# Kernel tuning notes

Measured on AMD Instinct MI355X. Metric: run time of the kernel, lower is better.

Reference implementation:

```python
import jax, jax.numpy as jnp
import numpy as np

B, L, C, H = 8, 2048, 1024, 16
HID = 4 * C


def _rope(x):
    # Faithful to source: rotation angle depends only on feature index (no position scaling).
    b, n, c = x.shape
    k_max = c // 2
    theta = 1.0 / (10000.0 ** (jnp.arange(k_max, dtype=jnp.float32) / k_max))
    cos_t, sin_t = jnp.cos(theta), jnp.sin(theta)
    xr = x.reshape(b, n, k_max, 2)
    re = xr[..., 0] * cos_t - xr[..., 1] * sin_t
    im = xr[..., 0] * sin_t + xr[..., 1] * cos_t
    return jnp.stack((re, im), axis=-1).reshape(b, n, c)


def _dwconv(x_bcl, w, bias):
    # depthwise conv1d, kernel 3, padding 1; w: (C,1,3)
    y = jax.lax.conv_general_dilated(
        x_bcl, w, (1,), [(1, 1)],
        dimension_numbers=('NCH', 'OIH', 'NCH'),
        feature_group_count=x_bcl.shape[1])
    return y + bias[None, :, None]


def _ln(x, g, b, eps=1e-5):
    mu = x.mean(-1, keepdims=True)
    var = ((x - mu) ** 2).mean(-1, keepdims=True)
    return (x - mu) * jax.lax.rsqrt(var + eps) * g + b


def _mlla_forward(x, cpe1_w, cpe1_b, norm1_g, norm1_b, in_w, in_b, actp_w, actp_b,
                  dwc_w, dwc_b, qk_w, qk_b, lepe_w, lepe_b, out_w, out_b,
                  cpe2_w, cpe2_b, norm2_g, norm2_b, fc1_w, fc1_b, fc2_w, fc2_b):
    b, n, c = x.shape
    h, d = H, c // H
    # cpe1 residual
    x = x + _dwconv(x.transpose(0, 2, 1), cpe1_w, cpe1_b).transpose(0, 2, 1)
    shortcut = x
    xn = _ln(x, norm1_g, norm1_b)
    act_res = jax.nn.silu(xn @ actp_w + actp_b)
    xi = xn @ in_w + in_b
    xi = jax.nn.silu(_dwconv(xi.transpose(0, 2, 1), dwc_w, dwc_b)).transpose(0, 2, 1)
    # linear attention with ELU+1 feature map and RoPE on q/k
    qk = xi @ qk_w + qk_b                       # (b,n,2c)
    q = jax.nn.elu(qk[..., :c]) + 1.0
    k = jax.nn.elu(qk[..., c:]) + 1.0
    q_rope = _rope(q).reshape(b, n, h, d).transpose(0, 2, 1, 3)  # (b,h,n,d)
    k_rope = _rope(k).reshape(b, n, h, d).transpose(0, 2, 1, 3)
    qh = q.reshape(b, n, h, d).transpose(0, 2, 1, 3)
    kh = k.reshape(b, n, h, d).transpose(0, 2, 1, 3)
    vh = xi.reshape(b, n, h, d).transpose(0, 2, 1, 3)
    k_mean = kh.mean(axis=2, keepdims=True)                      # (b,h,1,d)
    z = 1.0 / (jnp.einsum('bhnd,bhmd->bhnm', qh, k_mean) + 1e-6)  # (b,h,n,1)
    kv = jnp.einsum('bhnd,bhne->bhde', k_rope, vh) * (1.0 / n)   # (k*n^-0.5)^T @ (v*n^-0.5)
    attn = jnp.einsum('bhnd,bhde->bhne', q_rope, kv) * z         # (b,h,n,d)
    attn = attn.transpose(0, 2, 1, 3).reshape(b, n, c)
    v_bcl = vh.transpose(0, 2, 1, 3).reshape(b, n, c).transpose(0, 2, 1)
    attn = attn + _dwconv(v_bcl, lepe_w, lepe_b).transpose(0, 2, 1)
    # gated output projection + residual
    x = shortcut + (attn * act_res) @ out_w + out_b
    # cpe2 residual
    x = x + _dwconv(x.transpose(0, 2, 1), cpe2_w, cpe2_b).transpose(0, 2, 1)
    # MLP (exact GELU, as torch default)
    xn2 = _ln(x, norm2_g, norm2_b)
    mlp = jax.nn.gelu(xn2 @ fc1_w + fc1_b, approximate=False) @ fc2_w + fc2_b
    return x + mlp


def setup_inputs() -> dict:
    key = jax.random.key(0)
    ks = jax.random.split(key, 12)
    def nrm(k, shape, scale=0.02):
        return jax.random.normal(k, shape, jnp.float32) * scale
    return {
        'x': jax.random.normal(ks[0], (B, L, C), jnp.float32),
        'cpe1_w': nrm(ks[1], (C, 1, 3), 0.1), 'cpe1_b': jnp.zeros((C,), jnp.float32),
        'norm1_g': jnp.ones((C,), jnp.float32), 'norm1_b': jnp.zeros((C,), jnp.float32),
        'in_w': nrm(ks[2], (C, C)), 'in_b': jnp.zeros((C,), jnp.float32),
        'actp_w': nrm(ks[3], (C, C)), 'actp_b': jnp.zeros((C,), jnp.float32),
        'dwc_w': nrm(ks[4], (C, 1, 3), 0.1), 'dwc_b': jnp.zeros((C,), jnp.float32),
        'qk_w': nrm(ks[5], (C, 2 * C)), 'qk_b': jnp.zeros((2 * C,), jnp.float32),
        'lepe_w': nrm(ks[6], (C, 1, 3), 0.1), 'lepe_b': jnp.zeros((C,), jnp.float32),
        'out_w': nrm(ks[7], (C, C)), 'out_b': jnp.zeros((C,), jnp.float32),
        'cpe2_w': nrm(ks[8], (C, 1, 3), 0.1), 'cpe2_b': jnp.zeros((C,), jnp.float32),
        'norm2_g': jnp.ones((C,), jnp.float32), 'norm2_b': jnp.zeros((C,), jnp.float32),
        'fc1_w': nrm(ks[9], (C, HID)), 'fc1_b': jnp.zeros((HID,), jnp.float32),
        'fc2_w': nrm(ks[10], (HID, C)), 'fc2_b': jnp.zeros((C,), jnp.float32),
    }


def reference(x, cpe1_w, cpe1_b, norm1_g, norm1_b, in_w, in_b, actp_w, actp_b,
              dwc_w, dwc_b, qk_w, qk_b, lepe_w, lepe_b, out_w, out_b,
              cpe2_w, cpe2_b, norm2_g, norm2_b, fc1_w, fc1_b, fc2_w, fc2_b):
    return _mlla_forward(x, cpe1_w, cpe1_b, norm1_g, norm1_b, in_w, in_b, actp_w, actp_b,
                         dwc_w, dwc_b, qk_w, qk_b, lepe_w, lepe_b, out_w, out_b,
                         cpe2_w, cpe2_b, norm2_g, norm2_b, fc1_w, fc1_b, fc2_w, fc2_b)
```

## Files before the change

kernel.cpp:

```cpp
#include <hip/hip_runtime.h>
#include <hip/hip_bf16.h>
#include <cstdint>

#define B_    8
#define L_    2048
#define C_    1024
#define H_    16
#define D_    64
#define BL_   16384
#define C2_   2048
#define HID_  4096
#define KMAX_ 512

typedef unsigned short u16;
typedef unsigned int   u32;
typedef __attribute__((ext_vector_type(8))) short short8;
typedef __attribute__((ext_vector_type(4))) float f32x4;
typedef __attribute__((ext_vector_type(16))) float f32x16;

__device__ __forceinline__ u16 f2bf(float f){
  u32 u = __float_as_uint(f);
  u += 0x7fffu + ((u >> 16) & 1u);
  return (u16)(u >> 16);
}
__device__ __forceinline__ float bf2f(u16 v){
  return __uint_as_float(((u32)v) << 16);
}
__device__ __forceinline__ void gld16(const void* g, void* l){
  __builtin_amdgcn_global_load_lds((const __attribute__((address_space(1))) u32*)g,
                                   (__attribute__((address_space(3))) u32*)l, 16, 0, 0);
}

__global__ __launch_bounds__(256) void zerofill_kernel(float* __restrict__ p, int n){
  int i = blockIdx.x * 256 + threadIdx.x;
  if (i < n) p[i] = 0.f;
}

__global__ __launch_bounds__(256) void concat_bias_kernel(
    const float* __restrict__ b0, const float* __restrict__ b1, float* __restrict__ o){
  int i = blockIdx.x * 256 + threadIdx.x;
  if (i < C_) o[i] = b0[i];
  else if (i < C2_) o[i] = b1[i - C_];
}

__global__ void rope_table_kernel(float* __restrict__ cosS, float* __restrict__ sinS){
  int t = threadIdx.x;
  if (t < KMAX_){
    float th = powf(10000.f, -(float)t / (float)KMAX_);
    cosS[t] = cosf(th);
    sinS[t] = sinf(th);
  }
}

__global__ __launch_bounds__(256) void transpose_bf16_kernel(
    const float* __restrict__ in, u16* __restrict__ out, int R, int Ccol)
{
  __shared__ float tile[32][33];
  int tx = threadIdx.x & 31, ty = threadIdx.x >> 5;
  int c = blockIdx.x * 32 + tx;
  #pragma unroll
  for (int i = 0; i < 4; ++i){
    int r = blockIdx.y * 32 + ty + i * 8;
    tile[ty + i * 8][tx] = in[(size_t)r * Ccol + c];
  }
  __syncthreads();
  int rr = blockIdx.y * 32 + tx;
  #pragma unroll
  for (int i = 0; i < 4; ++i){
    int cc = blockIdx.x * 32 + ty + i * 8;
    out[(size_t)cc * R + rr] = f2bf(tile[tx][ty + i * 8]);
  }
}

template<typename T>
__global__ __launch_bounds__(256) void cpe_ln_kernel(
    const T* __restrict__ xin, const float* __restrict__ cw, const float* __restrict__ cb,
    const float* __restrict__ g,   const float* __restrict__ beta,
    u16* __restrict__ xout, u16* __restrict__ xnout)
{
  int bl = blockIdx.x;
  int l  = bl & (L_ - 1);
  const T* xr = xin + (size_t)bl * C_;
  int t = threadIdx.x;
  float vals[4];
  float s = 0.f, ss = 0.f;
  #pragma unroll
  for (int i = 0; i < 4; ++i){
    int c = t + i * 256;
    float xm = (l > 0)      ? (float)xr[c - C_] : 0.f;
    float x0 = (float)xr[c];
    float xp = (l < L_ - 1) ? (float)xr[c + C_] : 0.f;
    float v = x0 + xm * cw[c*3] + x0 * cw[c*3+1] + xp * cw[c*3+2] + cb[c];
    vals[i] = v; s += v; ss += v * v;
  }
  int lane = t & 63, w = t >> 6;
  #pragma unroll
  for (int o = 32; o > 0; o >>= 1){ s += __shfl_down(s, o); ss += __shfl_down(ss, o); }
  __shared__ float red[8];
  __shared__ float sh[2];
  if (lane == 0){ red[w] = s; red[4 + w] = ss; }
  __syncthreads();
  if (t == 0){
    float S  = red[0] + red[1] + red[2] + red[3];
    float SS = red[4] + red[5] + red[6] + red[7];
    float mu = S * (1.f / C_);
    float var = SS * (1.f / C_) - mu * mu;
    sh[0] = mu; sh[1] = rsqrtf(var + 1e-5f);
  }
  __syncthreads();
  float mu = sh[0], inv = sh[1];
  #pragma unroll
  for (int i = 0; i < 4; ++i){
    int c = t + i * 256;
    float xn = (vals[i] - mu) * inv * g[c] + beta[c];
    xout[(size_t)bl * C_ + c]  = f2bf(vals[i]);
    xnout[(size_t)bl * C_ + c] = f2bf(xn);
  }
}
template<> __global__ __launch_bounds__(256) void cpe_ln_kernel<u16>(
    const u16* __restrict__ xin, const float* __restrict__ cw, const float* __restrict__ cb,
    const float* __restrict__ g,   const float* __restrict__ beta,
    u16* __restrict__ xout, u16* __restrict__ xnout)
{
  int bl = blockIdx.x;
  int l  = bl & (L_ - 1);
  const u16* xr = xin + (size_t)bl * C_;
  int t = threadIdx.x;
  float vals[4];
  float s = 0.f, ss = 0.f;
  #pragma unroll
  for (int i = 0; i < 4; ++i){
    int c = t + i * 256;
    float xm = (l > 0)      ? bf2f(xr[c - C_]) : 0.f;
    float x0 = bf2f(xr[c]);
    float xp = (l < L_ - 1) ? bf2f(xr[c + C_]) : 0.f;
    float v = x0 + xm * cw[c*3] + x0 * cw[c*3+1] + xp * cw[c*3+2] + cb[c];
    vals[i] = v; s += v; ss += v * v;
  }
  int lane = t & 63, w = t >> 6;
  #pragma unroll
  for (int o = 32; o > 0; o >>= 1){ s += __shfl_down(s, o); ss += __shfl_down(ss, o); }
  __shared__ float red[8];
  __shared__ float sh[2];
  if (lane == 0){ red[w] = s; red[4 + w] = ss; }
  __syncthreads();
  if (t == 0){
    float S  = red[0] + red[1] + red[2] + red[3];
    float SS = red[4] + red[5] + red[6] + red[7];
    float mu = S * (1.f / C_);
    float var = SS * (1.f / C_) - mu * mu;
    sh[0] = mu; sh[1] = rsqrtf(var + 1e-5f);
  }
  __syncthreads();
  float mu = sh[0], inv = sh[1];
  #pragma unroll
  for (int i = 0; i < 4; ++i){
    int c = t + i * 256;
    float xn = (vals[i] - mu) * inv * g[c] + beta[c];
    xout[(size_t)bl * C_ + c]  = f2bf(vals[i]);
    xnout[(size_t)bl * C_ + c] = f2bf(xn);
  }
}

__global__ __launch_bounds__(256) void dwconv_silu_kernel(
    const u16* __restrict__ xin, const float* __restrict__ w, const float* __restrict__ bias,
    u16* __restrict__ xb)
{
  int bl = blockIdx.x;
  int l  = bl & (L_ - 1);
  const u16* xr = xin + (size_t)bl * C_;
  int t = threadIdx.x;
  #pragma unroll
  for (int i = 0; i < 4; ++i){
    int c = t + i * 256;
    float xm = (l > 0)      ? bf2f(xr[c - C_]) : 0.f;
    float x0 = bf2f(xr[c]);
    float xp = (l < L_ - 1) ? bf2f(xr[c + C_]) : 0.f;
    float v = xm * w[c*3] + x0 * w[c*3+1] + xp * w[c*3+2] + bias[c];
    v = v / (1.f + expf(-v));
    xb[(size_t)bl * C_ + c] = f2bf(v);
  }
}

__global__ __launch_bounds__(256) void colmean_kernel(
    const u16* __restrict__ qkb, float* __restrict__ kmean)
{
  int chunk = blockIdx.x, b = blockIdx.y;
  int l0 = chunk * 64;
  int t = threadIdx.x;
  #pragma unroll
  for (int i = 0; i < 4; ++i){
    int c = t + i * 256;
    float s = 0.f;
    for (int r = 0; r < 64; ++r)
      s += bf2f(qkb[((size_t)(b * L_ + l0 + r)) * C2_ + C_ + c]);
    atomicAdd(&kmean[b * C_ + c], s * (1.f / (float)L_));
  }
}

__global__ __launch_bounds__(256) void z_kernel(
    const u16* __restrict__ qkb, const float* __restrict__ kmean,
    float* __restrict__ zg)
{
  int idx = blockIdx.x * 256 + threadIdx.x;
  int row = idx >> 4, h = idx & 15;
  int b = row >> 11;
  const u32* qp = (const u32*)(qkb + (size_t)row * C2_ + h * 64);
  const float2* kp = (const float2*)(kmean + b * C_ + h * 64);
  float dot = 0.f;
  #pragma unroll
  for (int i = 0; i < 32; ++i){
    u32 q2 = qp[i]; float2 k2 = kp[i];
    dot += bf2f((u16)(q2 & 0xffff)) * k2.x + bf2f((u16)(q2 >> 16)) * k2.y;
  }
  zg[idx] = 1.f / (dot + 1e-6f);
}

__global__ __launch_bounds__(256) void kv_partial_kernel(
    const u16* __restrict__ qkb, const u16* __restrict__ xi,
    const float* __restrict__ cosS, const float* __restrict__ sinS,
    float* __restrict__ part)
{
  int bh = blockIdx.x, cy = blockIdx.y;
  int b = bh >> 4, h = bh & 15;
  __shared__ float kl[8][64];
  __shared__ float vl[8][64];
  int t = threadIdx.x;
  int rs = t >> 5, j = t & 31;
  int d  = t >> 2, e0 = (t & 3) << 4;
  float cj = cosS[h * 32 + j], sj = sinS[h * 32 + j];
  float acc[16];
  #pragma unroll
  for (int e = 0; e < 16; ++e) acc[e] = 0.f;
  int l0 = cy * 512;
  for (int it = 0; it < 64; ++it){
    int l = l0 + it * 8 + rs;
    u32 kp = *(const u32*)(qkb + ((size_t)(b * L_ + l)) * C2_ + C_ + h * 64 + 2 * j);
    float k0 = bf2f((u16)(kp & 0xffff)), k1 = bf2f((u16)(kp >> 16));
    kl[rs][2*j]   = k0 * cj - k1 * sj;
    kl[rs][2*j+1] = k0 * sj + k1 * cj;
    u32 vp = *(const u32*)(xi + ((size_t)(b * L_ + l)) * C_ + h * 64 + 2 * j);
    vl[rs][2*j]   = bf2f((u16)(vp & 0xffff));
    vl[rs][2*j+1] = bf2f((u16)(vp >> 16));
    __syncthreads();
    #pragma unroll
    for (int r = 0; r < 8; ++r){
      float kd = kl[r][d];
      #pragma unroll
      for (int e = 0; e < 16; ++e) acc[e] += kd * vl[r][e0 + e];
    }
    __syncthreads();
  }
  float* po = part + ((size_t)(bh * 4 + cy)) * 4096 + d * 64 + e0;
  #pragma unroll
  for (int e = 0; e < 16; ++e) po[e] = acc[e];
}

__global__ __launch_bounds__(256) void kv_reduce_kernel(
    const float* __restrict__ part, u16* __restrict__ kvb)
{
  int bh = blockIdx.x;
  int t = threadIdx.x;
  #pragma unroll
  for (int i = 0; i < 16; ++i){
    int o = t + i * 256;
    int d = o >> 6, e = o & 63;
    float s = 0.f;
    #pragma unroll
    for (int cy = 0; cy < 4; ++cy)
      s += part[((size_t)(bh * 4 + cy)) * 4096 + o];
    kvb[(size_t)bh * 4096 + e * 64 + d] = f2bf(s * (1.f / (float)L_));
  }
}

__global__ __launch_bounds__(256, 4) void attn_kernel(
    const u16* __restrict__ qkb, const u16* __restrict__ xi,
    const u16* __restrict__ kvb, const float* __restrict__ zg,
    const float* __restrict__ cosS, const float* __restrict__ sinS,
    const float* __restrict__ lw,  const float* __restrict__ lb,
    const u16* __restrict__ actres, u16* __restrict__ gout)
{
  int rc = blockIdx.x, b = blockIdx.y, h = blockIdx.z;
  __shared__ u16 qs[64 * 64];
  int t = threadIdx.x;
  int lane = t & 63, w = t >> 6;
  int bh = b * H_ + h;
  short8 bq[4][2];
  #pragma unroll
  for (int ni = 0; ni < 4; ++ni)
    #pragma unroll
    for (int kf = 0; kf < 2; ++kf)
      bq[ni][kf] = *(const short8*)(kvb + (size_t)bh * 4096 +
                     (ni * 16 + (lane & 15)) * 64 + kf * 32 + (lane >> 4) * 8);
  int js = t & 31;
  float cj = cosS[h * 32 + js], sj = sinS[h * 32 + js];
  float w0[4], w1[4], w2[4], bb[4];
  #pragma unroll
  for (int ni = 0; ni < 4; ++ni){
    int c = h * 64 + ni * 16 + (lane & 15);
    w0[ni] = lw[c*3]; w1[ni] = lw[c*3+1]; w2[ni] = lw[c*3+2]; bb[ni] = lb[c];
  }
  for (int ch = 0; ch < 2; ++ch){
    int n0 = rc * 128 + ch * 64;
    #pragma unroll
    for (int i = 0; i < 8; ++i){
      int id = t + i * 256;
      int r = id >> 5;
      u32 q2 = *(const u32*)(qkb + ((size_t)(b * L_ + n0 + r)) * C2_ + h * 64 + 2 * js);
      float q0 = bf2f((u16)(q2 & 0xffff)), q1 = bf2f((u16)(q2 >> 16));
      u32 pk = (u32)f2bf(q0 * cj - q1 * sj) | ((u32)f2bf(q0 * sj + q1 * cj) << 16);
      *(u32*)((char*)qs + r * 128 + ((4 * js) ^ ((r & 7) << 4))) = pk;
    }
    __syncthreads();
    int arow = w * 16 + (lane & 15);
    short8 af0 = *(const short8*)((char*)qs + arow * 128 + ((     (lane >> 4) * 16) ^ ((arow & 7) << 4)));
    short8 af1 = *(const short8*)((char*)qs + arow * 128 + ((64 + (lane >> 4) * 16) ^ ((arow & 7) << 4)));
    f32x4 acc[4] = {};
    #pragma unroll
    for (int ni = 0; ni < 4; ++ni){
      acc[ni] = __builtin_amdgcn_mfma_f32_16x16x32_bf16(af0, bq[ni][0], acc[ni], 0, 0, 0);
      acc[ni] = __builtin_amdgcn_mfma_f32_16x16x32_bf16(af1, bq[ni][1], acc[ni], 0, 0, 0);
    }
    #pragma unroll
    for (int ni = 0; ni < 4; ++ni){
      int c = h * 64 + ni * 16 + (lane & 15);
      #pragma unroll
      for (int r = 0; r < 4; ++r){
        int n = n0 + w * 16 + (lane >> 4) * 4 + r;
        size_t row = (size_t)b * L_ + n;
        float attnv = acc[ni][r] * zg[(row << 4) + h];
        float vm = (n > 0)      ? bf2f(xi[(row - 1) * C_ + c]) : 0.f;
        float v0 = bf2f(xi[row * C_ + c]);
        float vp = (n < L_ - 1) ? bf2f(xi[(row + 1) * C_ + c]) : 0.f;
        float gval = (attnv + vm * w0[ni] + v0 * w1[ni] + vp * w2[ni] + bb[ni]) * bf2f(actres[row * C_ + c]);
        gout[row * C_ + c] = f2bf(gval);
      }
    }
    __syncthreads();
  }
}

enum { EP_SILU = 0, EP_NONE = 1, EP_ELU1 = 2, EP_RES_BF = 3, EP_GELU = 4, EP_RES_F32 = 5, EP_ACTIN = 6 };

template<int EP>
__global__ __launch_bounds__(256) void gemm_bf16(
    const u16* __restrict__ A,
    const u16* __restrict__ Bt,
    const float* __restrict__ bias,
    const u16* __restrict__ res,
    float* __restrict__ outF, u16* __restrict__ outB, u16* __restrict__ outB2,
    int M, int N, int K)
{
  __shared__ u16 As[128 * 64];
  __shared__ u16 Bs[128 * 64];
  const int t = threadIdx.x;
  const int m0 = blockIdx.x * 128;
  const int n0 = blockIdx.y * 128;
  const int lane = t & 63, w = t >> 6;
  const int wm = (w >> 1) * 64, wn = (w & 1) * 64;
  f32x16 acc00 = {}, acc01 = {}, acc10 = {}, acc11 = {};
  const int ktiles = K >> 6;
  for (int kt = 0; kt < ktiles; ++kt){
    const u16* Ab = A  + (size_t)m0 * K + kt * 64;
    const u16* Bb = Bt + (size_t)n0 * K + kt * 64;
    #pragma unroll
    for (int i = 0; i < 4; ++i){
      int idx = t + i * 256;
      int row = idx >> 3, k8 = idx & 7;
      int srcoff = row * K + ((k8 * 8) ^ ((row & 7) << 3));
      int wb = (i * 256 + (t & 192)) * 8;
      gld16(Ab + srcoff, &As[wb]);
      gld16(Bb + srcoff, &Bs[wb]);
    }
    __syncthreads();
    const int rA0 = wm + (lane & 31), rA1 = rA0 + 32;
    const int rB0 = wn + (lane & 31), rB1 = rB0 + 32;
    const int sw = (lane & 7) << 3;
    #pragma unroll
    for (int ks = 0; ks < 4; ++ks){
      int kb = ks * 16 + ((lane >> 5) << 3);
      short8 a0 = *(const short8*)(&As[rA0 * 64 + (kb ^ sw)]);
      short8 a1 = *(const short8*)(&As[rA1 * 64 + (kb ^ sw)]);
      short8 b0 = *(const short8*)(&Bs[rB0 * 64 + (kb ^ sw)]);
      short8 b1 = *(const short8*)(&Bs[rB1 * 64 + (kb ^ sw)]);
      acc00 = __builtin_amdgcn_mfma_f32_32x32x16_bf16(a0, b0, acc00, 0, 0, 0);
      acc01 = __builtin_amdgcn_mfma_f32_32x32x16_bf16(a0, b1, acc01, 0, 0, 0);
      acc10 = __builtin_amdgcn_mfma_f32_32x32x16_bf16(a1, b0, acc10, 0, 0, 0);
      acc11 = __builtin_amdgcn_mfma_f32_32x32x16_bf16(a1, b1, acc11, 0, 0, 0);
    }
    __syncthreads();
  }
  const int rbase = (lane >> 5) << 2;
  #pragma unroll
  for (int mi = 0; mi < 2; ++mi){
    #pragma unroll
    for (int ni = 0; ni < 2; ++ni){
      const f32x16& a = (mi == 0) ? (ni == 0 ? acc00 : acc01) : (ni == 0 ? acc10 : acc11);
      int gn = n0 + wn + ni * 32 + (lane & 31);
      float bv = bias[gn];
      #pragma unroll
      for (int r = 0; r < 16; ++r){
        int gm = m0 + wm + mi * 32 + (r & 3) + ((r >> 2) << 3) + rbase;
        float v = a[r] + bv;
        size_t o = (size_t)gm * N + gn;
        if (EP == EP_SILU)      outB[o] = f2bf(v / (1.f + expf(-v)));
        else if (EP == EP_NONE) outB[o] = f2bf(v);
        else if (EP == EP_ELU1) outB[o] = f2bf((v > 0.f) ? (v + 1.f) : expf(v));
        else if (EP == EP_RES_BF) outB[o] = f2bf(v + bf2f(res[o]));
        else if (EP == EP_GELU){
          float u = v * (1.5957691f + 0.0713549f * v * v);
          outB[o] = f2bf(v / (1.f + expf(-u)));
        }
        else if (EP == EP_RES_F32) outF[o] = v + bf2f(res[o]);
        else if (EP == EP_ACTIN){
          int half = N >> 1;
          if (gn < half) outB[(size_t)gm * half + gn] = f2bf(v / (1.f + expf(-v)));
          else           outB2[(size_t)gm * half + gn - half] = f2bf(v);
        }
      }
    }
  }
}

extern "C" void kernel_launch(void* const* d_in, const int* in_sizes, int n_in,
                              void* d_out, int out_size, void* d_ws, size_t ws_size,
                              hipStream_t stream)
{
  const float* x       = (const float*)d_in[0];
  const float* cpe1_w  = (const float*)d_in[1];
  const float* cpe1_b  = (const float*)d_in[2];
  const float* norm1_g = (const float*)d_in[3];
  const float* norm1_b = (const float*)d_in[4];
  const float* in_w    = (const float*)d_in[5];
  const float* in_b    = (const float*)d_in[6];
  const float* actp_w  = (const float*)d_in[7];
  const float* actp_b  = (const float*)d_in[8];
  const float* dwc_w   = (const float*)d_in[9];
  const float* dwc_b   = (const float*)d_in[10];
  const float* qk_w    = (const float*)d_in[11];
  const float* qk_b    = (const float*)d_in[12];
  const float* lepe_w  = (const float*)d_in[13];
  const float* lepe_b  = (const float*)d_in[14];
  const float* out_w   = (const float*)d_in[15];
  const float* out_b   = (const float*)d_in[16];
  const float* cpe2_w  = (const float*)d_in[17];
  const float* cpe2_b  = (const float*)d_in[18];
  const float* norm2_g = (const float*)d_in[19];
  const float* norm2_b = (const float*)d_in[20];
  const float* fc1_w   = (const float*)d_in[21];
  const float* fc1_b   = (const float*)d_in[22];
  const float* fc2_w   = (const float*)d_in[23];
  const float* fc2_b   = (const float*)d_in[24];
  float* out = (float*)d_out;

  char* ws = (char*)d_ws;
  size_t off = 0;
  auto alloc = [&](size_t bytes) -> char* {
    char* p = ws + off;
    off = (off + bytes + 255) & ~(size_t)255;
    return p;
  };
  float* cosS   = (float*)alloc(KMAX_ * 4);
  float* sinS   = (float*)alloc(KMAX_ * 4);
  u16* wTai     = (u16*)alloc((size_t)2 * C_ * C_ * 2);
  u16* wTqk     = (u16*)alloc((size_t)C2_ * C_ * 2);
  u16* wTout    = (u16*)alloc((size_t)C_ * C_ * 2);
  u16* wTfc1    = (u16*)alloc((size_t)HID_ * C_ * 2);
  u16* wTfc2    = (u16*)alloc((size_t)C_ * HID_ * 2);
  float* biasAI = (float*)alloc((size_t)C2_ * 4);
  float* kmean  = (float*)alloc((size_t)B_ * C_ * 4);
  u16*   kvb    = (u16*)alloc((size_t)128 * 4096 * 2);
  float* kvpart = (float*)alloc((size_t)512 * 4096 * 4);
  float* zbuf   = (float*)alloc((size_t)BL_ * H_ * 4);
  u16* x1       = (u16*)alloc((size_t)BL_ * C_ * 2);
  u16* bufX     = (u16*)alloc((size_t)BL_ * C_ * 2);
  u16* bufY     = (u16*)alloc((size_t)BL_ * C_ * 2);
  u16* bufW     = (u16*)alloc((size_t)BL_ * C_ * 2);
  u16* bufQ     = (u16*)alloc((size_t)BL_ * C2_ * 2);
  size_t needed = off;
  if (ws_size < needed) return;

  u16* wTactp = wTai;
  u16* wTin   = wTai + (size_t)C_ * C_;
  u16* xi0 = bufQ;
  u16* qkb = bufQ;
  u16* x2  = bufQ;
  u16* xi  = bufW;
  u16* hb  = bufW;
  u16* actres = bufY;
  u16* x3  = bufY;

  rope_table_kernel<<<1, 512, 0, stream>>>(cosS, sinS);
  transpose_bf16_kernel<<<dim3(C_/32,  C_/32 ), 256, 0, stream>>>(actp_w, wTactp, C_,  C_);
  transpose_bf16_kernel<<<dim3(C_/32,  C_/32 ), 256, 0, stream>>>(in_w,   wTin,   C_,  C_);
  transpose_bf16_kernel<<<dim3(C2_/32, C_/32 ), 256, 0, stream>>>(qk_w,   wTqk,   C_,  C2_);
  transpose_bf16_kernel<<<dim3(C_/32,  C_/32 ), 256, 0, stream>>>(out_w,  wTout,  C_,  C_);
  transpose_bf16_kernel<<<dim3(HID_/32,C_/32 ), 256, 0, stream>>>(fc1_w,  wTfc1,  C_,  HID_);
  transpose_bf16_kernel<<<dim3(C_/32,  HID_/32), 256, 0, stream>>>(fc2_w,  wTfc2,  HID_, C_);
  concat_bias_kernel<<<C2_/256, 256, 0, stream>>>(actp_b, in_b, biasAI);
  zerofill_kernel<<<(B_*C_ + 255)/256, 256, 0, stream>>>(kmean, B_*C_);

  cpe_ln_kernel<float><<<BL_, 256, 0, stream>>>(x, cpe1_w, cpe1_b, norm1_g, norm1_b, x1, bufX);
  gemm_bf16<EP_ACTIN><<<dim3(BL_/128, C2_/128), 256, 0, stream>>>(
      bufX, wTai, biasAI, nullptr, nullptr, actres, xi0, BL_, C2_, C_);
  dwconv_silu_kernel<<<BL_, 256, 0, stream>>>(xi0, dwc_w, dwc_b, xi);
  gemm_bf16<EP_ELU1><<<dim3(BL_/128, C2_/128), 256, 0, stream>>>(
      xi, wTqk, qk_b, nullptr, nullptr, qkb, nullptr, BL_, C2_, C_);
  colmean_kernel<<<dim3(32, B_), 256, 0, stream>>>(qkb, kmean);
  z_kernel<<<BL_*H_/256, 256, 0, stream>>>(qkb, kmean, zbuf);
  kv_partial_kernel<<<dim3(128, 4), 256, 0, stream>>>(qkb, xi, cosS, sinS, kvpart);
  kv_reduce_kernel<<<128, 256, 0, stream>>>(kvpart, kvb);
  attn_kernel<<<dim3(16, B_, H_), 256, 0, stream>>>(
      qkb, xi, kvb, zbuf, cosS, sinS, lepe_w, lepe_b, actres, bufX);
  gemm_bf16<EP_RES_BF><<<dim3(BL_/128, C_/128), 256, 0, stream>>>(
      bufX, wTout, out_b, x1, nullptr, x2, nullptr, BL_, C_, C_);
  cpe_ln_kernel<u16><<<BL_, 256, 0, stream>>>(x2, cpe2_w, cpe2_b, norm2_g, norm2_b, x3, bufX);
  for (int m = 0; m < 4; ++m){
    size_t ro = (size_t)m * 4096;
    gemm_bf16<EP_GELU><<<dim3(32, HID_/128), 256, 0, stream>>>(
        bufX + ro * C_, wTfc1, fc1_b, nullptr, nullptr, hb, nullptr, 4096, HID_, C_);
    gemm_bf16<EP_RES_F32><<<dim3(32, C_/128), 256, 0, stream>>>(
        hb, wTfc2, fc2_b, x3 + ro * C_, out + ro * C_, nullptr, nullptr, 4096, C_, HID_);
  }
}
```

Before: 1.260 ms.

## Retune GEMM LDS swizzle, batch kv_partial rows, and enlarge MLP GEMM chunks

The GEMM's LDS XOR swizzle now mixes in higher row bits, and the B tile uses a different swizzle than the A tile, to reduce bank conflicts on the short8 reads. kv_partial stages 32 rows per barrier instead of 8, cutting the number of __syncthreads by four. The MLP is split into two chunks of 8192 rows instead of four of 4096, with the hidden buffer moved to the larger bufQ, giving bigger grids and fewer launches. Shared memory use in kv_partial grows, and the swizzle change must stay consistent between the global-to-LDS writes and the LDS reads.

```diff
diff --git a/kernel.cpp b/kernel.cpp
--- a/kernel.cpp
+++ b/kernel.cpp
@@ -30,6 +30,8 @@
   __builtin_amdgcn_global_load_lds((const __attribute__((address_space(1))) u32*)g,
                                    (__attribute__((address_space(3))) u32*)l, 16, 0, 0);
 }
+__device__ __forceinline__ int swzA(int row){ return ((row ^ (row >> 3)) & 7) << 3; }
+__device__ __forceinline__ int swzB(int row){ return ((((row ^ (row >> 3)) & 7) ^ 5)) << 3; }
 
 __global__ __launch_bounds__(256) void zerofill_kernel(float* __restrict__ p, int n){
   int i = blockIdx.x * 256 + threadIdx.x;
@@ -223,28 +225,32 @@
 {
   int bh = blockIdx.x, cy = blockIdx.y;
   int b = bh >> 4, h = bh & 15;
-  __shared__ float kl[8][64];
-  __shared__ float vl[8][64];
-  int t = threadIdx.x;
-  int rs = t >> 5, j = t & 31;
+  __shared__ float kl[32][64];
+  __shared__ float vl[32][64];
+  int t = threadIdx.x;
+  int rsb = t >> 5, j = t & 31;
   int d  = t >> 2, e0 = (t & 3) << 4;
   float cj = cosS[h * 32 + j], sj = sinS[h * 32 + j];
   float acc[16];
   #pragma unroll
   for (int e = 0; e < 16; ++e) acc[e] = 0.f;
   int l0 = cy * 512;
-  for (int it = 0; it < 64; ++it){
-    int l = l0 + it * 8 + rs;
-    u32 kp = *(const u32*)(qkb + ((size_t)(b * L_ + l)) * C2_ + C_ + h * 64 + 2 * j);
-    float k0 = bf2f((u16)(kp & 0xffff)), k1 = bf2f((u16)(kp >> 16));
-    kl[rs][2*j]   = k0 * cj - k1 * sj;
-    kl[rs][2*j+1] = k0 * sj + k1 * cj;
-    u32 vp = *(const u32*)(xi + ((size_t)(b * L_ + l)) * C_ + h * 64 + 2 * j);
-    vl[rs][2*j]   = bf2f((u16)(vp & 0xffff));
-    vl[rs][2*j+1] = bf2f((u16)(vp >> 16));
+  for (int it = 0; it < 16; ++it){
+    #pragma unroll
+    for (int rr = 0; rr < 4; ++rr){
+      int r = rsb + rr * 8;
+      int l = l0 + it * 32 + r;
+      u32 kp = *(const u32*)(qkb + ((size_t)(b * L_ + l)) * C2_ + C_ + h * 64 + 2 * j);
+      float k0 = bf2f((u16)(kp & 0xffff)), k1 = bf2f((u16)(kp >> 16));
+      kl[r][2*j]   = k0 * cj - k1 * sj;
+      kl[r][2*j+1] = k0 * sj + k1 * cj;
+      u32 vp = *(const u32*)(xi + ((size_t)(b * L_ + l)) * C_ + h * 64 + 2 * j);
+      vl[r][2*j]   = bf2f((u16)(vp & 0xffff));
+      vl[r][2*j+1] = bf2f((u16)(vp >> 16));
+    }
     __syncthreads();
     #pragma unroll
-    for (int r = 0; r < 8; ++r){
+    for (int r = 0; r < 32; ++r){
       float kd = kl[r][d];
       #pragma unroll
       for (int e = 0; e < 16; ++e) acc[e] += kd * vl[r][e0 + e];
@@ -367,22 +373,24 @@
     for (int i = 0; i < 4; ++i){
       int idx = t + i * 256;
       int row = idx >> 3, k8 = idx & 7;
-      int srcoff = row * K + ((k8 * 8) ^ ((row & 7) << 3));
+      int srcA = row * K + ((k8 * 8) ^ swzA(row));
+      int srcB = row * K + ((k8 * 8) ^ swzB(row));
       int wb = (i * 256 + (t & 192)) * 8;
-      gld16(Ab + srcoff, &As[wb]);
-      gld16(Bb + srcoff, &Bs[wb]);
+      gld16(Ab + srcA, &As[wb]);
+      gld16(Bb + srcB, &Bs[wb]);
     }
     __syncthreads();
     const int rA0 = wm + (lane & 31), rA1 = rA0 + 32;
     const int rB0 = wn + (lane & 31), rB1 = rB0 + 32;
-    const int sw = (lane & 7) << 3;
+    const int sA0 = swzA(rA0), sA1 = swzA(rA1);
+    const int sB0 = swzB(rB0), sB1 = swzB(rB1);
     #pragma unroll
     for (int ks = 0; ks < 4; ++ks){
       int kb = ks * 16 + ((lane >> 5) << 3);
-      short8 a0 = *(const short8*)(&As[rA0 * 64 + (kb ^ sw)]);
-      short8 a1 = *(const short8*)(&As[rA1 * 64 + (kb ^ sw)]);
-      short8 b0 = *(const short8*)(&Bs[rB0 * 64 + (kb ^ sw)]);
-      short8 b1 = *(const short8*)(&Bs[rB1 * 64 + (kb ^ sw)]);
+      short8 a0 = *(const short8*)(&As[rA0 * 64 + (kb ^ sA0)]);
+      short8 a1 = *(const short8*)(&As[rA1 * 64 + (kb ^ sA1)]);
+      short8 b0 = *(const short8*)(&Bs[rB0 * 64 + (kb ^ sB0)]);
+      short8 b1 = *(const short8*)(&Bs[rB1 * 64 + (kb ^ sB1)]);
       acc00 = __builtin_amdgcn_mfma_f32_32x32x16_bf16(a0, b0, acc00, 0, 0, 0);
       acc01 = __builtin_amdgcn_mfma_f32_32x32x16_bf16(a0, b1, acc01, 0, 0, 0);
       acc10 = __builtin_amdgcn_mfma_f32_32x32x16_bf16(a1, b0, acc10, 0, 0, 0);
@@ -485,8 +493,8 @@
   u16* xi0 = bufQ;
   u16* qkb = bufQ;
   u16* x2  = bufQ;
+  u16* hb  = bufQ;
   u16* xi  = bufW;
-  u16* hb  = bufW;
   u16* actres = bufY;
   u16* x3  = bufY;
 
@@ -515,11 +523,11 @@
   gemm_bf16<EP_RES_BF><<<dim3(BL_/128, C_/128), 256, 0, stream>>>(
       bufX, wTout, out_b, x1, nullptr, x2, nullptr, BL_, C_, C_);
   cpe_ln_kernel<u16><<<BL_, 256, 0, stream>>>(x2, cpe2_w, cpe2_b, norm2_g, norm2_b, x3, bufX);
-  for (int m = 0; m < 4; ++m){
-    size_t ro = (size_t)m * 4096;
-    gemm_bf16<EP_GELU><<<dim3(32, HID_/128), 256, 0, stream>>>(
-        bufX + ro * C_, wTfc1, fc1_b, nullptr, nullptr, hb, nullptr, 4096, HID_, C_);
-    gemm_bf16<EP_RES_F32><<<dim3(32, C_/128), 256, 0, stream>>>(
-        hb, wTfc2, fc2_b, x3 + ro * C_, out + ro * C_, nullptr, nullptr, 4096, C_, HID_);
-  }
-}
+  for (int m = 0; m < 2; ++m){
+    size_t ro = (size_t)m * 8192;
+    gemm_bf16<EP_GELU><<<dim3(64, HID_/128), 256, 0, stream>>>(
+        bufX + ro * C_, wTfc1, fc1_b, nullptr, nullptr, hb, nullptr, 8192, HID_, C_);
+    gemm_bf16<EP_RES_F32><<<dim3(64, C_/128), 256, 0, stream>>>(
+        hb, wTfc2, fc2_b, x3 + ro * C_, out + ro * C_, nullptr, nullptr, 8192, C_, HID_);
+  }
+}
```

Measured after the change: 1.175 ms. 6.8% less time.
